# Optimization experiments

Measured on AMD Instinct MI355X. Metric: run time of the kernel, lower is better.

Reference implementation:

```python
import jax, jax.numpy as jnp
import numpy as np

N, E, D = 100000, 640000, 128

def setup_inputs() -> dict:
    key = jax.random.key(0)
    ks = jax.random.split(key, 12)
    s = 1.0 / np.sqrt(D)
    sg = 1.0 / np.sqrt(2 * D)
    return {
        "nodes": jax.random.normal(ks[0], (N, D), jnp.float32),
        "globals_": jax.random.normal(ks[1], (1, D), jnp.float32),
        "senders": jax.random.randint(ks[2], (E,), 0, N, jnp.int32),
        "receivers": jax.random.randint(ks[3], (E,), 0, N, jnp.int32),
        "W1_w": jax.random.normal(ks[4], (D, D), jnp.float32) * s,
        "W1_b": jnp.zeros((D,), jnp.float32),
        "W2_w": jax.random.normal(ks[5], (D, D), jnp.float32) * s,
        "W2_b": jnp.zeros((D,), jnp.float32),
        "W3_w": jax.random.normal(ks[6], (D, D), jnp.float32) * s,
        "W3_b": jnp.zeros((D,), jnp.float32),
        "Wg_w": jax.random.normal(ks[7], (2 * D, D), jnp.float32) * sg,
        "Wg_b": jnp.zeros((D,), jnp.float32),
    }


def reference(nodes, globals_, senders, receivers,
              W1_w, W1_b, W2_w, W2_b, W3_w, W3_b, Wg_w, Wg_b):
    n = nodes.shape[0]
    # W1 skip-branch projection
    h = nodes @ W1_w + W1_b                              # [N, D]
    # GraphConvolution: W2 projection + symmetric-normalized sum aggregation
    conv = nodes @ W2_w + W2_b                           # [N, D]
    ones = jnp.ones(senders.shape, conv.dtype)
    send_deg = jax.ops.segment_sum(ones, senders, num_segments=n)
    recv_deg = jax.ops.segment_sum(ones, receivers, num_segments=n)
    conv = conv * jax.lax.rsqrt(jnp.maximum(send_deg, 1.0))[:, None]
    agg = jax.ops.segment_sum(conv[senders], receivers, num_segments=n)  # gather + scatter
    agg = agg * jax.lax.rsqrt(jnp.maximum(recv_deg, 1.0))[:, None]
    h = h + agg
    # global -> node broadcast (globals is not None)
    h = h + (globals_[0:1] @ W3_w + W3_b)
    h = jax.nn.relu(h)
    h = h + nodes                                        # residual
    # global update: aggregate nodes (sum over single graph) + gated residual
    an = jnp.sum(h, axis=0, keepdims=True)               # [1, D]
    g_new = globals_ + jax.nn.relu(jnp.concatenate([an, globals_], axis=-1) @ Wg_w + Wg_b)
    return h, g_new
```

## Files before the change

kernel.cpp:

```cpp
#include <hip/hip_runtime.h>

#define D 128
#define AGGB 2048
#define MAXDEG 16
#define OVFCAP 16384

typedef __attribute__((ext_vector_type(8))) short short8;
typedef __attribute__((ext_vector_type(4))) float floatx4;

__device__ inline void bf16split(float x, ushort& hi, ushort& lo) {
  unsigned u = __float_as_uint(x);
  unsigned rh = (u + 0x7FFFu + ((u >> 16) & 1u)) & 0xFFFF0000u;
  hi = (ushort)(rh >> 16);
  float fl = x - __uint_as_float(rh);
  unsigned ul = __float_as_uint(fl);
  lo = (ushort)((ul + 0x7FFFu + ((ul >> 16) & 1u)) >> 16);
}

__global__ void k_front(const int* __restrict__ snd, const int* __restrict__ rcv,
                        int* __restrict__ cs, int* __restrict__ cr,
                        int* __restrict__ srtp, int* __restrict__ ovf,
                        int* __restrict__ ovfn, int E, int nbE,
                        const float* __restrict__ g, const float* __restrict__ W3,
                        const float* __restrict__ b3, float* __restrict__ gvec,
                        const float* __restrict__ W1, const float* __restrict__ W2,
                        ushort* __restrict__ wt) {
  __shared__ float part[256];
  const int b = blockIdx.x;
  if (b < nbE) {
    const int e = b * 256 + threadIdx.x;
    if (e < E) {
      const int s = snd[e], r = rcv[e];
      atomicAdd(cs + s, 1);
      const int p = atomicAdd(cr + r, 1);
      if (p < MAXDEG) {
        srtp[r * MAXDEG + p] = s;
      } else {
        const int q = atomicAdd(ovfn, 1);
        if (q < OVFCAP) {
          ovf[2 * q] = r;
          ovf[2 * q + 1] = s;
        }
      }
    }
    return;
  }
  if (b == nbE) {
    const int j = threadIdx.x & 127, half = threadIdx.x >> 7;
    float acc = 0.f;
    for (int k = half * 64; k < half * 64 + 64; ++k)
      acc = fmaf(g[k], W3[k * D + j], acc);
    part[threadIdx.x] = acc;
    __syncthreads();
    if (threadIdx.x < D) gvec[j] = b3[j] + part[j] + part[j + 128];
    return;
  }
  const int id = (b - nbE - 1) * 256 + threadIdx.x;
  const int mat = id >> 14, idx = id & 16383;
  const int k = idx >> 7, nn = idx & 127;
  const float x = (mat ? W2 : W1)[k * D + nn];
  ushort hi, lo;
  bf16split(x, hi, lo);
  wt[(size_t)mat * 32768 + (size_t)nn * 128 + k] = hi;
  wt[(size_t)mat * 32768 + 16384 + (size_t)nn * 128 + k] = lo;
}

__global__ __launch_bounds__(256) void k_agg(
    const float* __restrict__ nodes, int* __restrict__ cnt_recv,
    const int* __restrict__ cnt_send, const int* __restrict__ srtp,
    const int* __restrict__ ovf, const int* __restrict__ ovfn,
    ushort* __restrict__ yh, ushort* __restrict__ yl, int n) {
  float* cf = (float*)cnt_recv;
  const int hw = threadIdx.x >> 5, ln = threadIdx.x & 31;
  const int ghw = blockIdx.x * 8 + hw;
  const int nhw = AGGB * 8;
  const int c0 = ln * 4;

  for (int r0 = ghw; r0 < n; r0 += 2 * nhw) {
    const int r1 = r0 + nhw;
    const bool has1 = r1 < n;
    const int dg0 = cnt_recv[r0];
    const int dg1 = has1 ? cnt_recv[r1] : 0;
    const int base0 = r0 * MAXDEG;
    const int base1 = (has1 ? r1 : 0) * MAXDEG;

    int idx0[8], idx1[8];
#pragma unroll
    for (int j = 0; j < 8; ++j) {
      const int raw0 = srtp[base0 + j];
      const int raw1 = srtp[base1 + j];
      idx0[j] = (j < dg0) ? raw0 : 0;
      idx1[j] = (j < dg1) ? raw1 : 0;
    }
    float4 g0[8], g1[8];
#pragma unroll
    for (int j = 0; j < 8; ++j)
      g0[j] = *(const float4*)(nodes + (size_t)idx0[j] * D + c0);
#pragma unroll
    for (int j = 0; j < 8; ++j)
      g1[j] = *(const float4*)(nodes + (size_t)idx1[j] * D + c0);
    float rs0[8], rs1[8];
#pragma unroll
    for (int j = 0; j < 8; ++j) {
      rs0[j] = (j < dg0) ? rsqrtf(fmaxf((float)cnt_send[idx0[j]], 1.f)) : 0.f;
      rs1[j] = (j < dg1) ? rsqrtf(fmaxf((float)cnt_send[idx1[j]], 1.f)) : 0.f;
    }

    float sx0 = 0.f, sy0 = 0.f, sz0 = 0.f, sw0 = 0.f, cs0 = 0.f;
    float sx1 = 0.f, sy1 = 0.f, sz1 = 0.f, sw1 = 0.f, cs1 = 0.f;
#pragma unroll
    for (int j = 0; j < 8; ++j) {
      sx0 = fmaf(rs0[j], g0[j].x, sx0);
      sy0 = fmaf(rs0[j], g0[j].y, sy0);
      sz0 = fmaf(rs0[j], g0[j].z, sz0);
      sw0 = fmaf(rs0[j], g0[j].w, sw0);
      cs0 += rs0[j];
      sx1 = fmaf(rs1[j], g1[j].x, sx1);
      sy1 = fmaf(rs1[j], g1[j].y, sy1);
      sz1 = fmaf(rs1[j], g1[j].z, sz1);
      sw1 = fmaf(rs1[j], g1[j].w, sw1);
      cs1 += rs1[j];
    }
    for (int i = 8; i < min(dg0, MAXDEG); ++i) {
      const int s = srtp[base0 + i];
      const float r = rsqrtf(fmaxf((float)cnt_send[s], 1.f));
      const float4 c = *(const float4*)(nodes + (size_t)s * D + c0);
      sx0 = fmaf(r, c.x, sx0); sy0 = fmaf(r, c.y, sy0);
      sz0 = fmaf(r, c.z, sz0); sw0 = fmaf(r, c.w, sw0);
      cs0 += r;
    }
    for (int i = 8; i < min(dg1, MAXDEG); ++i) {
      const int s = srtp[base1 + i];
      const float r = rsqrtf(fmaxf((float)cnt_send[s], 1.f));
      const float4 c = *(const float4*)(nodes + (size_t)s * D + c0);
      sx1 = fmaf(r, c.x, sx1); sy1 = fmaf(r, c.y, sy1);
      sz1 = fmaf(r, c.z, sz1); sw1 = fmaf(r, c.w, sw1);
      cs1 += r;
    }
    if (dg0 > MAXDEG) {
      const int novf = min(*ovfn, OVFCAP);
      for (int k2 = 0; k2 < novf; ++k2) {
        if (ovf[2 * k2] == r0) {
          const int s = ovf[2 * k2 + 1];
          const float r = rsqrtf(fmaxf((float)cnt_send[s], 1.f));
          const float4 c = *(const float4*)(nodes + (size_t)s * D + c0);
          sx0 = fmaf(r, c.x, sx0); sy0 = fmaf(r, c.y, sy0);
          sz0 = fmaf(r, c.z, sz0); sw0 = fmaf(r, c.w, sw0);
          cs0 += r;
        }
      }
    }
    if (dg1 > MAXDEG) {
      const int novf = min(*ovfn, OVFCAP);
      for (int k2 = 0; k2 < novf; ++k2) {
        if (ovf[2 * k2] == r1) {
          const int s = ovf[2 * k2 + 1];
          const float r = rsqrtf(fmaxf((float)cnt_send[s], 1.f));
          const float4 c = *(const float4*)(nodes + (size_t)s * D + c0);
          sx1 = fmaf(r, c.x, sx1); sy1 = fmaf(r, c.y, sy1);
          sz1 = fmaf(r, c.z, sz1); sw1 = fmaf(r, c.w, sw1);
          cs1 += r;
        }
      }
    }

    {
      const float rr = rsqrtf(fmaxf((float)dg0, 1.f));
      ushort h0, l0, h1, l1, h2, l2, h3, l3;
      bf16split(sx0 * rr, h0, l0);
      bf16split(sy0 * rr, h1, l1);
      bf16split(sz0 * rr, h2, l2);
      bf16split(sw0 * rr, h3, l3);
      *(ushort4*)(yh + (size_t)r0 * D + c0) = make_ushort4(h0, h1, h2, h3);
      *(ushort4*)(yl + (size_t)r0 * D + c0) = make_ushort4(l0, l1, l2, l3);
      if (ln == 0) cf[r0] = rr * cs0;
    }
    if (has1) {
      const float rr = rsqrtf(fmaxf((float)dg1, 1.f));
      ushort h0, l0, h1, l1, h2, l2, h3, l3;
      bf16split(sx1 * rr, h0, l0);
      bf16split(sy1 * rr, h1, l1);
      bf16split(sz1 * rr, h2, l2);
      bf16split(sw1 * rr, h3, l3);
      *(ushort4*)(yh + (size_t)r1 * D + c0) = make_ushort4(h0, h1, h2, h3);
      *(ushort4*)(yl + (size_t)r1 * D + c0) = make_ushort4(l0, l1, l2, l3);
      if (ln == 0) cf[r1] = rr * cs1;
    }
  }
}

__global__ __launch_bounds__(256, 4) void k_gemm(
    const float* __restrict__ A, const ushort* __restrict__ yh,
    const ushort* __restrict__ yl, const ushort* __restrict__ wt,
    const float* __restrict__ b1, const float* __restrict__ b2,
    const float* __restrict__ gvec, const float* __restrict__ cf,
    float* __restrict__ outH, float* __restrict__ an, int n) {
  __shared__ ushort As[2 * 4 * 2560];
  const int t = threadIdx.x;
  const int row0 = blockIdx.x * 64;
  const int lane = t & 63, w = t >> 6;
  const int m = lane & 15, quad = lane >> 4;

  floatx4 acc[4][2];
#pragma unroll
  for (int i = 0; i < 4; ++i)
#pragma unroll
    for (int j = 0; j < 2; ++j) acc[i][j] = (floatx4)0.f;

  const int srow = t >> 2, ko = (t & 3) * 8;
  const int grow = min(row0 + srow, n - 1);
  const float* Ag = A + (size_t)grow * D + ko;
  const ushort* yhb = yh + (size_t)grow * D + ko;
  const ushort* ylb = yl + (size_t)grow * D + ko;
  const int sa = srow * 40 + ko;

  float4 f0, f1;
  uint4 r2, r3;
#define LOADP(p)                                  \
  {                                               \
    f0 = *(const float4*)(Ag + (p) * 32);         \
    f1 = *(const float4*)(Ag + (p) * 32 + 4);     \
    r2 = *(const uint4*)(yhb + (p) * 32);         \
    r3 = *(const uint4*)(ylb + (p) * 32);         \
  }
#define STOREB(buf)                                                        \
  {                                                                        \
    ushort h0, l0, h1, l1, h2, l2, h3, l3;                                 \
    ushort* Bp = &As[(buf) * 10240];                                       \
    bf16split(f0.x, h0, l0); bf16split(f0.y, h1, l1);                      \
    bf16split(f0.z, h2, l2); bf16split(f0.w, h3, l3);                      \
    *(ushort4*)&Bp[sa] = make_ushort4(h0, h1, h2, h3);                     \
    *(ushort4*)&Bp[2560 + sa] = make_ushort4(l0, l1, l2, l3);              \
    bf16split(f1.x, h0, l0); bf16split(f1.y, h1, l1);                      \
    bf16split(f1.z, h2, l2); bf16split(f1.w, h3, l3);                      \
    *(ushort4*)&Bp[sa + 4] = make_ushort4(h0, h1, h2, h3);                 \
    *(ushort4*)&Bp[2560 + sa + 4] = make_ushort4(l0, l1, l2, l3);          \
    *(uint4*)&Bp[5120 + sa] = r2;                                          \
    *(uint4*)&Bp[7680 + sa] = r3;                                          \
  }

  LOADP(0);
  STOREB(0);
  LOADP(1);
  __syncthreads();

  for (int p = 0; p < 4; ++p) {
    if (p < 3) STOREB((p + 1) & 1);
    if (p < 2) LOADP(p + 2);
    const ushort* Ab = &As[(p & 1) * 10240];
#pragma unroll
    for (int j = 0; j < 2; ++j) {
      const ushort* g1 = wt + (size_t)(w * 32 + j * 16 + m) * 128 + p * 32 + quad * 8;
      const short8 w1h = *(const short8*)g1;
      const short8 w1l = *(const short8*)(g1 + 16384);
      const short8 w2h = *(const short8*)(g1 + 32768);
      const short8 w2l = *(const short8*)(g1 + 49152);
#pragma unroll
      for (int i = 0; i < 4; ++i) {
        const int r = (i * 16 + m) * 40 + quad * 8;
        const short8 a1h = *(const short8*)&Ab[r];
        const short8 a1l = *(const short8*)&Ab[2560 + r];
        const short8 a2h = *(const short8*)&Ab[5120 + r];
        const short8 a2l = *(const short8*)&Ab[7680 + r];
        floatx4 c = acc[i][j];
        c = __builtin_amdgcn_mfma_f32_16x16x32_bf16(a1h, w1h, c, 0, 0, 0);
        c = __builtin_amdgcn_mfma_f32_16x16x32_bf16(a1h, w1l, c, 0, 0, 0);
        c = __builtin_amdgcn_mfma_f32_16x16x32_bf16(a1l, w1h, c, 0, 0, 0);
        c = __builtin_amdgcn_mfma_f32_16x16x32_bf16(a2h, w2h, c, 0, 0, 0);
        c = __builtin_amdgcn_mfma_f32_16x16x32_bf16(a2h, w2l, c, 0, 0, 0);
        c = __builtin_amdgcn_mfma_f32_16x16x32_bf16(a2l, w2h, c, 0, 0, 0);
        acc[i][j] = c;
      }
    }
    __syncthreads();
  }
#undef LOADP
#undef STOREB

  float bb[2], b2c[2];
#pragma unroll
  for (int j = 0; j < 2; ++j) {
    const int col = w * 32 + j * 16 + m;
    bb[j] = b1[col] + gvec[col];
    b2c[j] = b2[col];
  }
  float asum[2] = {0.f, 0.f};
#pragma unroll
  for (int i = 0; i < 4; ++i)
#pragma unroll
    for (int pp = 0; pp < 4; ++pp) {
      const int rg = row0 + i * 16 + quad * 4 + pp;
      if (rg >= n) continue;
      const float crv = cf[rg];
#pragma unroll
      for (int j = 0; j < 2; ++j) {
        const int col = w * 32 + j * 16 + m;
        float v = acc[i][j][pp] + bb[j] + crv * b2c[j];
        v = fmaxf(v, 0.f) + A[(size_t)rg * D + col];
        outH[(size_t)rg * D + col] = v;
        asum[j] += v;
      }
    }
#pragma unroll
  for (int j = 0; j < 2; ++j) {
    float v = asum[j];
    v += __shfl_xor(v, 16);
    v += __shfl_xor(v, 32);
    if (lane < 16) atomicAdd(an + w * 32 + j * 16 + m, v);
  }
}

__global__ void k_gupdate(const float* __restrict__ an, const float* __restrict__ g,
                          const float* __restrict__ Wg, const float* __restrict__ bg,
                          float* __restrict__ gout) {
  __shared__ float part[256];
  const int j = threadIdx.x & 127, half = threadIdx.x >> 7;
  float acc = 0.f;
  if (half == 0) {
    for (int k = 0; k < D; ++k) acc = fmaf(an[k], Wg[k * D + j], acc);
  } else {
    for (int k = 0; k < D; ++k) acc = fmaf(g[k], Wg[(D + k) * D + j], acc);
  }
  part[threadIdx.x] = acc;
  __syncthreads();
  if (threadIdx.x < D)
    gout[j] = g[j] + fmaxf(bg[j] + part[j] + part[j + 128], 0.f);
}

extern "C" void kernel_launch(void* const* d_in, const int* in_sizes, int n_in,
                              void* d_out, int out_size, void* d_ws, size_t ws_size,
                              hipStream_t stream) {
  const float* nodes = (const float*)d_in[0];
  const float* globals_ = (const float*)d_in[1];
  const int* senders = (const int*)d_in[2];
  const int* receivers = (const int*)d_in[3];
  const float* W1_w = (const float*)d_in[4];
  const float* W1_b = (const float*)d_in[5];
  const float* W2_w = (const float*)d_in[6];
  const float* W2_b = (const float*)d_in[7];
  const float* W3_w = (const float*)d_in[8];
  const float* W3_b = (const float*)d_in[9];
  const float* Wg_w = (const float*)d_in[10];
  const float* Wg_b = (const float*)d_in[11];
  const int N = in_sizes[0] / D;
  const int E = in_sizes[2];
  const int nbE = (E + 255) / 256;

  float* h = (float*)d_out;
  float* gout = h + (size_t)N * D;

  float* ws = (float*)d_ws;
  ushort* yh = (ushort*)ws;
  ushort* yl = yh + (size_t)N * D;
  int* cnt_send = (int*)(yl + (size_t)N * D);
  int* cnt_recv = cnt_send + N;
  float* an = (float*)(cnt_recv + N);
  int* ovfn = (int*)(an + D);
  float* gvec = (float*)(ovfn + 64);
  int* srtp = (int*)(gvec + D);
  int* ovf = srtp + (size_t)N * MAXDEG;
  ushort* wt = (ushort*)(ovf + 2 * OVFCAP);

  (void)hipMemsetAsync(cnt_send, 0, (size_t)(2 * N + D + 64) * sizeof(int), stream);

  hipLaunchKernelGGL(k_front, dim3(nbE + 1 + 128), dim3(256), 0, stream,
                     senders, receivers, cnt_send, cnt_recv, srtp, ovf, ovfn,
                     E, nbE, globals_, W3_w, W3_b, gvec, W1_w, W2_w, wt);
  hipLaunchKernelGGL(k_agg, dim3(AGGB), dim3(256), 0, stream,
                     nodes, cnt_recv, cnt_send, srtp, ovf, ovfn, yh, yl, N);
  hipLaunchKernelGGL(k_gemm, dim3((N + 63) / 64), dim3(256), 0, stream,
                     nodes, yh, yl, wt, W1_b, W2_b, gvec,
                     (const float*)cnt_recv, h, an, N);
  hipLaunchKernelGGL(k_gupdate, dim3(1), dim3(256), 0, stream, an, globals_,
                     Wg_w, Wg_b, gout);
}
```

Before: 350.2 us.

## Overlap W1 projection GEMM with edge counting and split GEMM into two passes

```diff
diff --git a/kernel.cpp b/kernel.cpp
--- a/kernel.cpp
+++ b/kernel.cpp
@@ -1,7 +1,7 @@
 #include <hip/hip_runtime.h>
 
 #define D 128
-#define AGGB 2048
+#define AGGB 3136
 #define MAXDEG 16
 #define OVFCAP 16384
 
@@ -17,35 +17,26 @@
   lo = (ushort)((ul + 0x7FFFu + ((ul >> 16) & 1u)) >> 16);
 }
 
-__global__ void k_front(const int* __restrict__ snd, const int* __restrict__ rcv,
-                        int* __restrict__ cs, int* __restrict__ cr,
-                        int* __restrict__ srtp, int* __restrict__ ovf,
-                        int* __restrict__ ovfn, int E, int nbE,
-                        const float* __restrict__ g, const float* __restrict__ W3,
-                        const float* __restrict__ b3, float* __restrict__ gvec,
-                        const float* __restrict__ W1, const float* __restrict__ W2,
-                        ushort* __restrict__ wt) {
-  __shared__ float part[256];
+__device__ inline void place_edge(int s, int r, int p, int* __restrict__ srtp,
+                                  int* __restrict__ ovf, int* __restrict__ ovfn) {
+  if (p < MAXDEG) {
+    srtp[r * MAXDEG + p] = s;
+  } else {
+    const int q = atomicAdd(ovfn, 1);
+    if (q < OVFCAP) {
+      ovf[2 * q] = r;
+      ovf[2 * q + 1] = s;
+    }
+  }
+}
+
+__global__ void k_prep(const float* __restrict__ g, const float* __restrict__ W3,
+                       const float* __restrict__ b3, float* __restrict__ gvec,
+                       const float* __restrict__ W1, const float* __restrict__ W2,
+                       ushort* __restrict__ wt) {
   const int b = blockIdx.x;
-  if (b < nbE) {
-    const int e = b * 256 + threadIdx.x;
-    if (e < E) {
-      const int s = snd[e], r = rcv[e];
-      atomicAdd(cs + s, 1);
-      const int p = atomicAdd(cr + r, 1);
-      if (p < MAXDEG) {
-        srtp[r * MAXDEG + p] = s;
-      } else {
-        const int q = atomicAdd(ovfn, 1);
-        if (q < OVFCAP) {
-          ovf[2 * q] = r;
-          ovf[2 * q + 1] = s;
-        }
-      }
-    }
-    return;
-  }
-  if (b == nbE) {
+  if (b == 0) {
+    __shared__ float part[256];
     const int j = threadIdx.x & 127, half = threadIdx.x >> 7;
     float acc = 0.f;
     for (int k = half * 64; k < half * 64 + 64; ++k)
@@ -55,7 +46,7 @@
     if (threadIdx.x < D) gvec[j] = b3[j] + part[j] + part[j + 128];
     return;
   }
-  const int id = (b - nbE - 1) * 256 + threadIdx.x;
+  const int id = (b - 1) * 256 + threadIdx.x;
   const int mat = id >> 14, idx = id & 16383;
   const int k = idx >> 7, nn = idx & 127;
   const float x = (mat ? W2 : W1)[k * D + nn];
@@ -63,6 +54,118 @@
   bf16split(x, hi, lo);
   wt[(size_t)mat * 32768 + (size_t)nn * 128 + k] = hi;
   wt[(size_t)mat * 32768 + 16384 + (size_t)nn * 128 + k] = lo;
+}
+
+__global__ __launch_bounds__(256, 6) void k_eg(
+    const int* __restrict__ snd, const int* __restrict__ rcv,
+    int* __restrict__ cs, int* __restrict__ cr, int* __restrict__ srtp,
+    int* __restrict__ ovf, int* __restrict__ ovfn, int E, int nbE4,
+    const float* __restrict__ A, const ushort* __restrict__ wt,
+    float* __restrict__ h1, int n) {
+  const int b = blockIdx.x, t = threadIdx.x;
+  if (b < nbE4) {
+    const int e0 = b * 1024 + t * 4;
+    if (e0 + 3 < E) {
+      const int4 s4 = *(const int4*)(snd + e0);
+      const int4 r4 = *(const int4*)(rcv + e0);
+      atomicAdd(cs + s4.x, 1);
+      atomicAdd(cs + s4.y, 1);
+      atomicAdd(cs + s4.z, 1);
+      atomicAdd(cs + s4.w, 1);
+      const int p0 = atomicAdd(cr + r4.x, 1);
+      const int p1 = atomicAdd(cr + r4.y, 1);
+      const int p2 = atomicAdd(cr + r4.z, 1);
+      const int p3 = atomicAdd(cr + r4.w, 1);
+      place_edge(s4.x, r4.x, p0, srtp, ovf, ovfn);
+      place_edge(s4.y, r4.y, p1, srtp, ovf, ovfn);
+      place_edge(s4.z, r4.z, p2, srtp, ovf, ovfn);
+      place_edge(s4.w, r4.w, p3, srtp, ovf, ovfn);
+    } else {
+      for (int e = e0; e < E && e < e0 + 4; ++e) {
+        const int s = snd[e], r = rcv[e];
+        atomicAdd(cs + s, 1);
+        place_edge(s, r, atomicAdd(cr + r, 1), srtp, ovf, ovfn);
+      }
+    }
+    return;
+  }
+  __shared__ ushort As[2 * 2 * 2560];
+  const int row0 = (b - nbE4) * 64;
+  const int lane = t & 63, w = t >> 6;
+  const int m = lane & 15, quad = lane >> 4;
+
+  floatx4 acc[4][2];
+#pragma unroll
+  for (int i = 0; i < 4; ++i)
+#pragma unroll
+    for (int j = 0; j < 2; ++j) acc[i][j] = (floatx4)0.f;
+
+  const int srow = t >> 2, ko = (t & 3) * 8;
+  const int grow = min(row0 + srow, n - 1);
+  const float* Ag = A + (size_t)grow * D + ko;
+  const int sa = srow * 40 + ko;
+
+  float4 f0, f1;
+#define LOADP(p)                              \
+  {                                           \
+    f0 = *(const float4*)(Ag + (p) * 32);     \
+    f1 = *(const float4*)(Ag + (p) * 32 + 4); \
+  }
+#define STOREB(buf)                                               \
+  {                                                               \
+    ushort h0, l0, h1_, l1_, h2, l2, h3, l3;                      \
+    ushort* Bp = &As[(buf) * 5120];                               \
+    bf16split(f0.x, h0, l0); bf16split(f0.y, h1_, l1_);           \
+    bf16split(f0.z, h2, l2); bf16split(f0.w, h3, l3);             \
+    *(ushort4*)&Bp[sa] = make_ushort4(h0, h1_, h2, h3);           \
+    *(ushort4*)&Bp[2560 + sa] = make_ushort4(l0, l1_, l2, l3);    \
+    bf16split(f1.x, h0, l0); bf16split(f1.y, h1_, l1_);           \
+    bf16split(f1.z, h2, l2); bf16split(f1.w, h3, l3);             \
+    *(ushort4*)&Bp[sa + 4] = make_ushort4(h0, h1_, h2, h3);       \
+    *(ushort4*)&Bp[2560 + sa + 4] = make_ushort4(l0, l1_, l2, l3);\
+  }
+
+  LOADP(0);
+  STOREB(0);
+  LOADP(1);
+  __syncthreads();
+
+  for (int p = 0; p < 4; ++p) {
+    if (p < 3) STOREB((p + 1) & 1);
+    if (p < 2) LOADP(p + 2);
+    const ushort* Ab = &As[(p & 1) * 5120];
+#pragma unroll
+    for (int j = 0; j < 2; ++j) {
+      const ushort* g1 = wt + (size_t)(w * 32 + j * 16 + m) * 128 + p * 32 + quad * 8;
+      const short8 w1h = *(const short8*)g1;
+      const short8 w1l = *(const short8*)(g1 + 16384);
+#pragma unroll
+      for (int i = 0; i < 4; ++i) {
+        const int r = (i * 16 + m) * 40 + quad * 8;
+        const short8 a1h = *(const short8*)&Ab[r];
+        const short8 a1l = *(const short8*)&Ab[2560 + r];
+        floatx4 c = acc[i][j];
+        c = __builtin_amdgcn_mfma_f32_16x16x32_bf16(a1h, w1h, c, 0, 0, 0);
+        c = __builtin_amdgcn_mfma_f32_16x16x32_bf16(a1h, w1l, c, 0, 0, 0);
+        c = __builtin_amdgcn_mfma_f32_16x16x32_bf16(a1l, w1h, c, 0, 0, 0);
+        acc[i][j] = c;
+      }
+    }
+    __syncthreads();
+  }
+#undef LOADP
+#undef STOREB
+
+#pragma unroll
+  for (int i = 0; i < 4; ++i)
+#pragma unroll
+    for (int pp = 0; pp < 4; ++pp) {
+      const int rg = row0 + i * 16 + quad * 4 + pp;
+      if (rg >= n) continue;
+#pragma unroll
+      for (int j = 0; j < 2; ++j)
+        h1[(size_t)rg * D + w * 32 + j * 16 + m] = acc[i][j][pp];
+    }
 }
 
 __global__ __launch_bounds__(256) void k_agg(
@@ -84,13 +187,16 @@
     const int base0 = r0 * MAXDEG;
     const int base1 = (has1 ? r1 : 0) * MAXDEG;
 
-    int idx0[8], idx1[8];
+    const int4 qa0 = *(const int4*)(srtp + base0);
+    const int4 qb0 = *(const int4*)(srtp + base0 + 4);
+    const int4 qa1 = *(const int4*)(srtp + base1);
+    const int4 qb1 = *(const int4*)(srtp + base1 + 4);
+    int idx0[8] = {qa0.x, qa0.y, qa0.z, qa0.w, qb0.x, qb0.y, qb0.z, qb0.w};
+    int idx1[8] = {qa1.x, qa1.y, qa1.z, qa1.w, qb1.x, qb1.y, qb1.z, qb1.w};
 #pragma unroll
     for (int j = 0; j < 8; ++j) {
-      const int raw0 = srtp[base0 + j];
-      const int raw1 = srtp[base1 + j];
-      idx0[j] = (j < dg0) ? raw0 : 0;
-      idx1[j] = (j < dg1) ? raw1 : 0;
+      idx0[j] = (j < dg0) ? idx0[j] : 0;
+      idx1[j] = (j < dg1) ? idx1[j] : 0;
     }
     float4 g0[8], g1[8];
 #pragma unroll
@@ -189,13 +295,13 @@
   }
 }
 
-__global__ __launch_bounds__(256, 4) void k_gemm(
+__global__ __launch_bounds__(256, 6) void k_gemm2(
     const float* __restrict__ A, const ushort* __restrict__ yh,
     const ushort* __restrict__ yl, const ushort* __restrict__ wt,
     const float* __restrict__ b1, const float* __restrict__ b2,
     const float* __restrict__ gvec, const float* __restrict__ cf,
-    float* __restrict__ outH, float* __restrict__ an, int n) {
-  __shared__ ushort As[2 * 4 * 2560];
+    float* hio, float* __restrict__ an, int n) {
+  __shared__ ushort As[2 * 2 * 2560];
   const int t = threadIdx.x;
   const int row0 = blockIdx.x * 64;
   const int lane = t & 63, w = t >> 6;
@@ -209,34 +315,21 @@
 
   const int srow = t >> 2, ko = (t & 3) * 8;
   const int grow = min(row0 + srow, n - 1);
-  const float* Ag = A + (size_t)grow * D + ko;
   const ushort* yhb = yh + (size_t)grow * D + ko;
   const ushort* ylb = yl + (size_t)grow * D + ko;
   const int sa = srow * 40 + ko;
 
-  float4 f0, f1;
   uint4 r2, r3;
-#define LOADP(p)                                  \
-  {                                               \
-    f0 = *(const float4*)(Ag + (p) * 32);         \
-    f1 = *(const float4*)(Ag + (p) * 32 + 4);     \
-    r2 = *(const uint4*)(yhb + (p) * 32);         \
-    r3 = *(const uint4*)(ylb + (p) * 32);         \
-  }
-#define STOREB(buf)                                                        \
-  {                                                                        \
-    ushort h0, l0, h1, l1, h2, l2, h3, l3;                                 \
-    ushort* Bp = &As[(buf) * 10240];                                       \
-    bf16split(f0.x, h0, l0); bf16split(f0.y, h1, l1);                      \
-    bf16split(f0.z, h2, l2); bf16split(f0.w, h3, l3);                      \
-    *(ushort4*)&Bp[sa] = make_ushort4(h0, h1, h2, h3);                     \
-    *(ushort4*)&Bp[2560 + sa] = make_ushort4(l0, l1, l2, l3);              \
-    bf16split(f1.x, h0, l0); bf16split(f1.y, h1, l1);                      \
-    bf16split(f1.z, h2, l2); bf16split(f1.w, h3, l3);                      \
-    *(ushort4*)&Bp[sa + 4] = make_ushort4(h0, h1, h2, h3);                 \
-    *(ushort4*)&Bp[2560 + sa + 4] = make_ushort4(l0, l1, l2, l3);          \
-    *(uint4*)&Bp[5120 + sa] = r2;                                          \
-    *(uint4*)&Bp[7680 + sa] = r3;                                          \
+#define LOADP(p)                          \
+  {                                       \
+    r2 = *(const uint4*)(yhb + (p) * 32); \
+    r3 = *(const uint4*)(ylb + (p) * 32); \
+  }
+#define STOREB(buf)                 \
+  {                                 \
+    ushort* Bp = &As[(buf) * 5120]; \
+    *(uint4*)&Bp[sa] = r2;          \
+    *(uint4*)&Bp[2560 + sa] = r3;   \
   }
 
   LOADP(0);
@@ -247,25 +340,19 @@
   for (int p = 0; p < 4; ++p) {
     if (p < 3) STOREB((p + 1) & 1);
     if (p < 2) LOADP(p + 2);
-    const ushort* Ab = &As[(p & 1) * 10240];
+    const ushort* Ab = &As[(p & 1) * 5120];
 #pragma unroll
     for (int j = 0; j < 2; ++j) {
-      const ushort* g1 = wt + (size_t)(w * 32 + j * 16 + m) * 128 + p * 32 + quad * 8;
-      const short8 w1h = *(const short8*)g1;
-      const short8 w1l = *(const short8*)(g1 + 16384);
-      const short8 w2h = *(const short8*)(g1 + 32768);
-      const short8 w2l = *(const short8*)(g1 + 49152);
+      const ushort* g2 =
+          wt + 32768 + (size_t)(w * 32 + j * 16 + m) * 128 + p * 32 + quad * 8;
+      const short8 w2h = *(const short8*)g2;
+      const short8 w2l = *(const short8*)(g2 + 16384);
 #pragma unroll
       for (int i = 0; i < 4; ++i) {
         const int r = (i * 16 + m) * 40 + quad * 8;
-        const short8 a1h = *(const short8*)&Ab[r];
-        const short8 a1l = *(const short8*)&Ab[2560 + r];
-        const short8 a2h = *(const short8*)&Ab[5120 + r];
-        const short8 a2l = *(const short8*)&Ab[7680 + r];
+        const short8 a2h = *(const short8*)&Ab[r];
+        const short8 a2l = *(const short8*)&Ab[2560 + r];
         floatx4 c = acc[i][j];
-        c = __builtin_amdgcn_mfma_f32_16x16x32_bf16(a1h, w1h, c, 0, 0, 0);
-        c = __builtin_amdgcn_mfma_f32_16x16x32_bf16(a1h, w1l, c, 0, 0, 0);
-        c = __builtin_amdgcn_mfma_f32_16x16x32_bf16(a1l, w1h, c, 0, 0, 0);
         c = __builtin_amdgcn_mfma_f32_16x16x32_bf16(a2h, w2h, c, 0, 0, 0);
         c = __builtin_amdgcn_mfma_f32_16x16x32_bf16(a2h, w2l, c, 0, 0, 0);
         c = __builtin_amdgcn_mfma_f32_16x16x32_bf16(a2l, w2h, c, 0, 0, 0);
@@ -295,9 +382,9 @@
 #pragma unroll
       for (int j = 0; j < 2; ++j) {
         const int col = w * 32 + j * 16 + m;
-        float v = acc[i][j][pp] + bb[j] + crv * b2c[j];
+        float v = acc[i][j][pp] + bb[j] + crv * b2c[j] + hio[(size_t)rg * D + col];
         v = fmaxf(v, 0.f) + A[(size_t)rg * D + col];
-        outH[(size_t)rg * D + col] = v;
+        hio[(size_t)rg * D + col] = v;
         asum[j] += v;
       }
     }
@@ -344,7 +431,8 @@
   const float* Wg_b = (const float*)d_in[11];
   const int N = in_sizes[0] / D;
   const int E = in_sizes[2];
-  const int nbE = (E + 255) / 256;
+  const int nbE4 = (E + 1023) / 1024;
+  const int NG = (N + 63) / 64;
 
   float* h = (float*)d_out;
   float* gout = h + (size_t)N * D;
@@ -363,12 +451,14 @@
 
   (void)hipMemsetAsync(cnt_send, 0, (size_t)(2 * N + D + 64) * sizeof(int), stream);
 
-  hipLaunchKernelGGL(k_front, dim3(nbE + 1 + 128), dim3(256), 0, stream,
+  hipLaunchKernelGGL(k_prep, dim3(129), dim3(256), 0, stream,
+                     globals_, W3_w, W3_b, gvec, W1_w, W2_w, wt);
+  hipLaunchKernelGGL(k_eg, dim3(nbE4 + NG), dim3(256), 0, stream,
                      senders, receivers, cnt_send, cnt_recv, srtp, ovf, ovfn,
-                     E, nbE, globals_, W3_w, W3_b, gvec, W1_w, W2_w, wt);
+                     E, nbE4, nodes, wt, h, N);
   hipLaunchKernelGGL(k_agg, dim3(AGGB), dim3(256), 0, stream,
                      nodes, cnt_recv, cnt_send, srtp, ovf, ovfn, yh, yl, N);
-  hipLaunchKernelGGL(k_gemm, dim3((N + 63) / 64), dim3(256), 0, stream,
+  hipLaunchKernelGGL(k_gemm2, dim3(NG), dim3(256), 0, stream,
                      nodes, yh, yl, wt, W1_b, W2_b, gvec,
                      (const float*)cnt_recv, h, an, N);
   hipLaunchKernelGGL(k_gupdate, dim3(1), dim3(256), 0, stream, an, globals_,
```

Result: slower. 376.5 us (+7.5%).

## Fuse neighbor aggregation into GEMM tile kernel and vectorize edge binning

Applied to the files above, without the earlier changes.

```diff
diff --git a/kernel.cpp b/kernel.cpp
--- a/kernel.cpp
+++ b/kernel.cpp
@@ -1,7 +1,6 @@
 #include <hip/hip_runtime.h>
 
 #define D 128
-#define AGGB 2048
 #define MAXDEG 16
 #define OVFCAP 16384
 
@@ -17,45 +16,66 @@
   lo = (ushort)((ul + 0x7FFFu + ((ul >> 16) & 1u)) >> 16);
 }
 
+__device__ inline void place_edge(int s, int r, int p, int* __restrict__ srtp,
+                                  int* __restrict__ ovf, int* __restrict__ ovfn) {
+  if (p < MAXDEG) {
+    srtp[r * MAXDEG + p] = s;
+  } else {
+    const int q = atomicAdd(ovfn, 1);
+    if (q < OVFCAP) {
+      ovf[2 * q] = r;
+      ovf[2 * q + 1] = s;
+    }
+  }
+}
+
 __global__ void k_front(const int* __restrict__ snd, const int* __restrict__ rcv,
                         int* __restrict__ cs, int* __restrict__ cr,
                         int* __restrict__ srtp, int* __restrict__ ovf,
-                        int* __restrict__ ovfn, int E, int nbE,
+                        int* __restrict__ ovfn, int E, int nbE4,
                         const float* __restrict__ g, const float* __restrict__ W3,
                         const float* __restrict__ b3, float* __restrict__ gvec,
                         const float* __restrict__ W1, const float* __restrict__ W2,
                         ushort* __restrict__ wt) {
-  __shared__ float part[256];
-  const int b = blockIdx.x;
-  if (b < nbE) {
-    const int e = b * 256 + threadIdx.x;
-    if (e < E) {
-      const int s = snd[e], r = rcv[e];
-      atomicAdd(cs + s, 1);
-      const int p = atomicAdd(cr + r, 1);
-      if (p < MAXDEG) {
-        srtp[r * MAXDEG + p] = s;
-      } else {
-        const int q = atomicAdd(ovfn, 1);
-        if (q < OVFCAP) {
-          ovf[2 * q] = r;
-          ovf[2 * q + 1] = s;
-        }
+  const int b = blockIdx.x, t = threadIdx.x;
+  if (b < nbE4) {
+    const int e0 = b * 1024 + t * 4;
+    if (e0 + 3 < E) {
+      const int4 s4 = *(const int4*)(snd + e0);
+      const int4 r4 = *(const int4*)(rcv + e0);
+      atomicAdd(cs + s4.x, 1);
+      atomicAdd(cs + s4.y, 1);
+      atomicAdd(cs + s4.z, 1);
+      atomicAdd(cs + s4.w, 1);
+      const int p0 = atomicAdd(cr + r4.x, 1);
+      const int p1 = atomicAdd(cr + r4.y, 1);
+      const int p2 = atomicAdd(cr + r4.z, 1);
+      const int p3 = atomicAdd(cr + r4.w, 1);
+      place_edge(s4.x, r4.x, p0, srtp, ovf, ovfn);
+      place_edge(s4.y, r4.y, p1, srtp, ovf, ovfn);
+      place_edge(s4.z, r4.z, p2, srtp, ovf, ovfn);
+      place_edge(s4.w, r4.w, p3, srtp, ovf, ovfn);
+    } else {
+      for (int e = e0; e < E && e < e0 + 4; ++e) {
+        const int s = snd[e], r = rcv[e];
+        atomicAdd(cs + s, 1);
+        place_edge(s, r, atomicAdd(cr + r, 1), srtp, ovf, ovfn);
       }
     }
     return;
   }
-  if (b == nbE) {
-    const int j = threadIdx.x & 127, half = threadIdx.x >> 7;
+  if (b == nbE4) {
+    __shared__ float part[256];
+    const int j = t & 127, half = t >> 7;
     float acc = 0.f;
     for (int k = half * 64; k < half * 64 + 64; ++k)
       acc = fmaf(g[k], W3[k * D + j], acc);
-    part[threadIdx.x] = acc;
+    part[t] = acc;
     __syncthreads();
-    if (threadIdx.x < D) gvec[j] = b3[j] + part[j] + part[j + 128];
+    if (t < D) gvec[j] = b3[j] + part[j] + part[j + 128];
     return;
   }
-  const int id = (b - nbE - 1) * 256 + threadIdx.x;
+  const int id = (b - nbE4 - 1) * 256 + t;
   const int mat = id >> 14, idx = id & 16383;
   const int k = idx >> 7, nn = idx & 127;
   const float x = (mat ? W2 : W1)[k * D + nn];
@@ -65,203 +85,176 @@
   wt[(size_t)mat * 32768 + 16384 + (size_t)nn * 128 + k] = lo;
 }
 
-__global__ __launch_bounds__(256) void k_agg(
-    const float* __restrict__ nodes, int* __restrict__ cnt_recv,
-    const int* __restrict__ cnt_send, const int* __restrict__ srtp,
+__global__ __launch_bounds__(256, 3) void k_ag2(
+    const float* __restrict__ nodes, const int* __restrict__ cr,
+    const int* __restrict__ cs, const int* __restrict__ srtp,
     const int* __restrict__ ovf, const int* __restrict__ ovfn,
-    ushort* __restrict__ yh, ushort* __restrict__ yl, int n) {
-  float* cf = (float*)cnt_recv;
-  const int hw = threadIdx.x >> 5, ln = threadIdx.x & 31;
-  const int ghw = blockIdx.x * 8 + hw;
-  const int nhw = AGGB * 8;
-  const int c0 = ln * 4;
-
-  for (int r0 = ghw; r0 < n; r0 += 2 * nhw) {
-    const int r1 = r0 + nhw;
-    const bool has1 = r1 < n;
-    const int dg0 = cnt_recv[r0];
-    const int dg1 = has1 ? cnt_recv[r1] : 0;
-    const int base0 = r0 * MAXDEG;
-    const int base1 = (has1 ? r1 : 0) * MAXDEG;
-
-    int idx0[8], idx1[8];
-#pragma unroll
-    for (int j = 0; j < 8; ++j) {
-      const int raw0 = srtp[base0 + j];
-      const int raw1 = srtp[base1 + j];
-      idx0[j] = (j < dg0) ? raw0 : 0;
-      idx1[j] = (j < dg1) ? raw1 : 0;
-    }
-    float4 g0[8], g1[8];
-#pragma unroll
-    for (int j = 0; j < 8; ++j)
-      g0[j] = *(const float4*)(nodes + (size_t)idx0[j] * D + c0);
-#pragma unroll
-    for (int j = 0; j < 8; ++j)
-      g1[j] = *(const float4*)(nodes + (size_t)idx1[j] * D + c0);
-    float rs0[8], rs1[8];
-#pragma unroll
-    for (int j = 0; j < 8; ++j) {
-      rs0[j] = (j < dg0) ? rsqrtf(fmaxf((float)cnt_send[idx0[j]], 1.f)) : 0.f;
-      rs1[j] = (j < dg1) ? rsqrtf(fmaxf((float)cnt_send[idx1[j]], 1.f)) : 0.f;
-    }
-
-    float sx0 = 0.f, sy0 = 0.f, sz0 = 0.f, sw0 = 0.f, cs0 = 0.f;
-    float sx1 = 0.f, sy1 = 0.f, sz1 = 0.f, sw1 = 0.f, cs1 = 0.f;
-#pragma unroll
-    for (int j = 0; j < 8; ++j) {
-      sx0 = fmaf(rs0[j], g0[j].x, sx0);
-      sy0 = fmaf(rs0[j], g0[j].y, sy0);
-      sz0 = fmaf(rs0[j], g0[j].z, sz0);
-      sw0 = fmaf(rs0[j], g0[j].w, sw0);
-      cs0 += rs0[j];
-      sx1 = fmaf(rs1[j], g1[j].x, sx1);
-      sy1 = fmaf(rs1[j], g1[j].y, sy1);
-      sz1 = fmaf(rs1[j], g1[j].z, sz1);
-      sw1 = fmaf(rs1[j], g1[j].w, sw1);
-      cs1 += rs1[j];
-    }
-    for (int i = 8; i < min(dg0, MAXDEG); ++i) {
-      const int s = srtp[base0 + i];
-      const float r = rsqrtf(fmaxf((float)cnt_send[s], 1.f));
-      const float4 c = *(const float4*)(nodes + (size_t)s * D + c0);
-      sx0 = fmaf(r, c.x, sx0); sy0 = fmaf(r, c.y, sy0);
-      sz0 = fmaf(r, c.z, sz0); sw0 = fmaf(r, c.w, sw0);
-      cs0 += r;
-    }
-    for (int i = 8; i < min(dg1, MAXDEG); ++i) {
-      const int s = srtp[base1 + i];
-      const float r = rsqrtf(fmaxf((float)cnt_send[s], 1.f));
-      const float4 c = *(const float4*)(nodes + (size_t)s * D + c0);
-      sx1 = fmaf(r, c.x, sx1); sy1 = fmaf(r, c.y, sy1);
-      sz1 = fmaf(r, c.z, sz1); sw1 = fmaf(r, c.w, sw1);
-      cs1 += r;
-    }
-    if (dg0 > MAXDEG) {
-      const int novf = min(*ovfn, OVFCAP);
-      for (int k2 = 0; k2 < novf; ++k2) {
-        if (ovf[2 * k2] == r0) {
-          const int s = ovf[2 * k2 + 1];
-          const float r = rsqrtf(fmaxf((float)cnt_send[s], 1.f));
-          const float4 c = *(const float4*)(nodes + (size_t)s * D + c0);
-          sx0 = fmaf(r, c.x, sx0); sy0 = fmaf(r, c.y, sy0);
-          sz0 = fmaf(r, c.z, sz0); sw0 = fmaf(r, c.w, sw0);
-          cs0 += r;
-        }
-      }
-    }
-    if (dg1 > MAXDEG) {
-      const int novf = min(*ovfn, OVFCAP);
-      for (int k2 = 0; k2 < novf; ++k2) {
-        if (ovf[2 * k2] == r1) {
-          const int s = ovf[2 * k2 + 1];
-          const float r = rsqrtf(fmaxf((float)cnt_send[s], 1.f));
-          const float4 c = *(const float4*)(nodes + (size_t)s * D + c0);
-          sx1 = fmaf(r, c.x, sx1); sy1 = fmaf(r, c.y, sy1);
-          sz1 = fmaf(r, c.z, sz1); sw1 = fmaf(r, c.w, sw1);
-          cs1 += r;
-        }
-      }
-    }
-
-    {
-      const float rr = rsqrtf(fmaxf((float)dg0, 1.f));
-      ushort h0, l0, h1, l1, h2, l2, h3, l3;
-      bf16split(sx0 * rr, h0, l0);
-      bf16split(sy0 * rr, h1, l1);
-      bf16split(sz0 * rr, h2, l2);
-      bf16split(sw0 * rr, h3, l3);
-      *(ushort4*)(yh + (size_t)r0 * D + c0) = make_ushort4(h0, h1, h2, h3);
-      *(ushort4*)(yl + (size_t)r0 * D + c0) = make_ushort4(l0, l1, l2, l3);
-      if (ln == 0) cf[r0] = rr * cs0;
-    }
-    if (has1) {
-      const float rr = rsqrtf(fmaxf((float)dg1, 1.f));
-      ushort h0, l0, h1, l1, h2, l2, h3, l3;
-      bf16split(sx1 * rr, h0, l0);
-      bf16split(sy1 * rr, h1, l1);
-      bf16split(sz1 * rr, h2, l2);
-      bf16split(sw1 * rr, h3, l3);
-      *(ushort4*)(yh + (size_t)r1 * D + c0) = make_ushort4(h0, h1, h2, h3);
-      *(ushort4*)(yl + (size_t)r1 * D + c0) = make_ushort4(l0, l1, l2, l3);
-      if (ln == 0) cf[r1] = rr * cs1;
-    }
-  }
-}
-
-__global__ __launch_bounds__(256, 4) void k_gemm(
-    const float* __restrict__ A, const ushort* __restrict__ yh,
-    const ushort* __restrict__ yl, const ushort* __restrict__ wt,
-    const float* __restrict__ b1, const float* __restrict__ b2,
-    const float* __restrict__ gvec, const float* __restrict__ cf,
-    float* __restrict__ outH, float* __restrict__ an, int n) {
-  __shared__ ushort As[2 * 4 * 2560];
+    const ushort* __restrict__ wt, const float* __restrict__ b1,
+    const float* __restrict__ b2, const float* __restrict__ gvec,
+    float* __restrict__ h, float* __restrict__ an, int n) {
+  __shared__ ushort As[4 * 5120];
+  __shared__ float cfl[32];
   const int t = threadIdx.x;
-  const int row0 = blockIdx.x * 64;
+  const int row0 = blockIdx.x * 32;
+
+  {
+    const int hw = t >> 5, ln = t & 31;
+    const int c0 = ln * 4;
+    const int sl = ln >> 3;
+    const int kk = (ln & 7) * 4;
+    const int sb = sl * 1280 + kk;
+
+    for (int it = 0; it < 2; ++it) {
+      const int lrA = hw + it * 8;
+      const int lrB = lrA + 16;
+      const int rA = row0 + lrA, rB = row0 + lrB;
+      const bool hasA = rA < n, hasB = rB < n;
+      const int dgA = hasA ? cr[rA] : 0;
+      const int dgB = hasB ? cr[rB] : 0;
+      const int baseA = (hasA ? rA : 0) * MAXDEG;
+      const int baseB = (hasB ? rB : 0) * MAXDEG;
+
+      const int4 qa0 = *(const int4*)(srtp + baseA);
+      const int4 qb0 = *(const int4*)(srtp + baseA + 4);
+      const int4 qa1 = *(const int4*)(srtp + baseB);
+      const int4 qb1 = *(const int4*)(srtp + baseB + 4);
+      int idxA[8] = {qa0.x, qa0.y, qa0.z, qa0.w, qb0.x, qb0.y, qb0.z, qb0.w};
+      int idxB[8] = {qa1.x, qa1.y, qa1.z, qa1.w, qb1.x, qb1.y, qb1.z, qb1.w};
+#pragma unroll
+      for (int j = 0; j < 8; ++j) {
+        idxA[j] = (j < dgA) ? idxA[j] : 0;
+        idxB[j] = (j < dgB) ? idxB[j] : 0;
+      }
+      float4 gA[8], gB[8];
+#pragma unroll
+      for (int j = 0; j < 8; ++j)
+        gA[j] = *(const float4*)(nodes + (size_t)idxA[j] * D + c0);
+#pragma unroll
+      for (int j = 0; j < 8; ++j)
+        gB[j] = *(const float4*)(nodes + (size_t)idxB[j] * D + c0);
+      const float4 ndA = hasA ? *(const float4*)(nodes + (size_t)rA * D + c0)
+                              : make_float4(0.f, 0.f, 0.f, 0.f);
+      const float4 ndB = hasB ? *(const float4*)(nodes + (size_t)rB * D + c0)
+                              : make_float4(0.f, 0.f, 0.f, 0.f);
+      float rsA[8], rsB[8];
+#pragma unroll
+      for (int j = 0; j < 8; ++j) {
+        rsA[j] = (j < dgA) ? rsqrtf(fmaxf((float)cs[idxA[j]], 1.f)) : 0.f;
+        rsB[j] = (j < dgB) ? rsqrtf(fmaxf((float)cs[idxB[j]], 1.f)) : 0.f;
+      }
+      float sxA = 0.f, syA = 0.f, szA = 0.f, swA = 0.f, csA = 0.f;
+      float sxB = 0.f, syB = 0.f, szB = 0.f, swB = 0.f, csB = 0.f;
+#pragma unroll
+      for (int j = 0; j < 8; ++j) {
+        sxA = fmaf(rsA[j], gA[j].x, sxA);
+        syA = fmaf(rsA[j], gA[j].y, syA);
+        szA = fmaf(rsA[j], gA[j].z, szA);
+        swA = fmaf(rsA[j], gA[j].w, swA);
+        csA += rsA[j];
+        sxB = fmaf(rsB[j], gB[j].x, sxB);
+        syB = fmaf(rsB[j], gB[j].y, syB);
+        szB = fmaf(rsB[j], gB[j].z, szB);
+        swB = fmaf(rsB[j], gB[j].w, swB);
+        csB += rsB[j];
+      }
+      for (int i = 8; i < min(dgA, MAXDEG); ++i) {
+        const int s = srtp[baseA + i];
+        const float r = rsqrtf(fmaxf((float)cs[s], 1.f));
+        const float4 c = *(const float4*)(nodes + (size_t)s * D + c0);
+        sxA = fmaf(r, c.x, sxA); syA = fmaf(r, c.y, syA);
+        szA = fmaf(r, c.z, szA); swA = fmaf(r, c.w, swA);
+        csA += r;
+      }
+      for (int i = 8; i < min(dgB, MAXDEG); ++i) {
+        const int s = srtp[baseB + i];
+        const float r = rsqrtf(fmaxf((float)cs[s], 1.f));
+        const float4 c = *(const float4*)(nodes + (size_t)s * D + c0);
+        sxB = fmaf(r, c.x, sxB); syB = fmaf(r, c.y, syB);
+        szB = fmaf(r, c.z, szB); swB = fmaf(r, c.w, swB);
+        csB += r;
+      }
+      if (dgA > MAXDEG) {
+        const int novf = min(*ovfn, OVFCAP);
+        for (int k2 = 0; k2 < novf; ++k2)
+          if (ovf[2 * k2] == rA) {
+            const int s = ovf[2 * k2 + 1];
+            const float r = rsqrtf(fmaxf((float)cs[s], 1.f));
+            const float4 c = *(const float4*)(nodes + (size_t)s * D + c0);
+            sxA = fmaf(r, c.x, sxA); syA = fmaf(r, c.y, syA);
+            szA = fmaf(r, c.z, szA); swA = fmaf(r, c.w, swA);
+            csA += r;
+          }
+      }
+      if (dgB > MAXDEG) {
+        const int novf = min(*ovfn, OVFCAP);
+        for (int k2 = 0; k2 < novf; ++k2)
+          if (ovf[2 * k2] == rB) {
+            const int s = ovf[2 * k2 + 1];
+            const float r = rsqrtf(fmaxf((float)cs[s], 1.f));
+            const float4 c = *(const float4*)(nodes + (size_t)s * D + c0);
+            sxB = fmaf(r, c.x, sxB); syB = fmaf(r, c.y, syB);
+            szB = fmaf(r, c.z, szB); swB = fmaf(r, c.w, swB);
+            csB += r;
+          }
+      }
+      if (hasA) {
+        const float rr = rsqrtf(fmaxf((float)dgA, 1.f));
+        ushort h0, l0, h1, l1, h2, l2, h3, l3;
+        const int a = sb + lrA * 40;
+        bf16split(ndA.x, h0, l0); bf16split(ndA.y, h1, l1);
+        bf16split(ndA.z, h2, l2); bf16split(ndA.w, h3, l3);
+        *(ushort4*)&As[a] = make_ushort4(h0, h1, h2, h3);
+        *(ushort4*)&As[5120 + a] = make_ushort4(l0, l1, l2, l3);
+        bf16split(sxA * rr, h0, l0); bf16split(syA * rr, h1, l1);
+        bf16split(szA * rr, h2, l2); bf16split(swA * rr, h3, l3);
+        *(ushort4*)&As[10240 + a] = make_ushort4(h0, h1, h2, h3);
+        *(ushort4*)&As[15360 + a] = make_ushort4(l0, l1, l2, l3);
+        if (ln == 0) cfl[lrA] = rr * csA;
+      }
+      if (hasB) {
+        const float rr = rsqrtf(fmaxf((float)dgB, 1.f));
+        ushort h0, l0, h1, l1, h2, l2, h3, l3;
+        const int a = sb + lrB * 40;
+        bf16split(ndB.x, h0, l0); bf16split(ndB.y, h1, l1);
+        bf16split(ndB.z, h2, l2); bf16split(ndB.w, h3, l3);
+        *(ushort4*)&As[a] = make_ushort4(h0, h1, h2, h3);
+        *(ushort4*)&As[5120 + a] = make_ushort4(l0, l1, l2, l3);
+        bf16split(sxB * rr, h0, l0); bf16split(syB * rr, h1, l1);
+        bf16split(szB * rr, h2, l2); bf16split(swB * rr, h3, l3);
+        *(ushort4*)&As[10240 + a] = make_ushort4(h0, h1, h2, h3);
+        *(ushort4*)&As[15360 + a] = make_ushort4(l0, l1, l2, l3);
+        if (ln == 0) cfl[lrB] = rr * csB;
+      }
+    }
+  }
+  __syncthreads();
+
   const int lane = t & 63, w = t >> 6;
   const int m = lane & 15, quad = lane >> 4;
 
-  floatx4 acc[4][2];
-#pragma unroll
-  for (int i = 0; i < 4; ++i)
+  floatx4 acc[2][2];
+#pragma unroll
+  for (int i = 0; i < 2; ++i)
 #pragma unroll
     for (int j = 0; j < 2; ++j) acc[i][j] = (floatx4)0.f;
 
-  const int srow = t >> 2, ko = (t & 3) * 8;
-  const int grow = min(row0 + srow, n - 1);
-  const float* Ag = A + (size_t)grow * D + ko;
-  const ushort* yhb = yh + (size_t)grow * D + ko;
-  const ushort* ylb = yl + (size_t)grow * D + ko;
-  const int sa = srow * 40 + ko;
-
-  float4 f0, f1;
-  uint4 r2, r3;
-#define LOADP(p)                                  \
-  {                                               \
-    f0 = *(const float4*)(Ag + (p) * 32);         \
-    f1 = *(const float4*)(Ag + (p) * 32 + 4);     \
-    r2 = *(const uint4*)(yhb + (p) * 32);         \
-    r3 = *(const uint4*)(ylb + (p) * 32);         \
-  }
-#define STOREB(buf)                                                        \
-  {                                                                        \
-    ushort h0, l0, h1, l1, h2, l2, h3, l3;                                 \
-    ushort* Bp = &As[(buf) * 10240];                                       \
-    bf16split(f0.x, h0, l0); bf16split(f0.y, h1, l1);                      \
-    bf16split(f0.z, h2, l2); bf16split(f0.w, h3, l3);                      \
-    *(ushort4*)&Bp[sa] = make_ushort4(h0, h1, h2, h3);                     \
-    *(ushort4*)&Bp[2560 + sa] = make_ushort4(l0, l1, l2, l3);              \
-    bf16split(f1.x, h0, l0); bf16split(f1.y, h1, l1);                      \
-    bf16split(f1.z, h2, l2); bf16split(f1.w, h3, l3);                      \
-    *(ushort4*)&Bp[sa + 4] = make_ushort4(h0, h1, h2, h3);                 \
-    *(ushort4*)&Bp[2560 + sa + 4] = make_ushort4(l0, l1, l2, l3);          \
-    *(uint4*)&Bp[5120 + sa] = r2;                                          \
-    *(uint4*)&Bp[7680 + sa] = r3;                                          \
-  }
-
-  LOADP(0);
-  STOREB(0);
-  LOADP(1);
-  __syncthreads();
-
+#pragma unroll
   for (int p = 0; p < 4; ++p) {
-    if (p < 3) STOREB((p + 1) & 1);
-    if (p < 2) LOADP(p + 2);
-    const ushort* Ab = &As[(p & 1) * 10240];
 #pragma unroll
     for (int j = 0; j < 2; ++j) {
-      const ushort* g1 = wt + (size_t)(w * 32 + j * 16 + m) * 128 + p * 32 + quad * 8;
+      const ushort* g1 =
+          wt + (size_t)(w * 32 + j * 16 + m) * 128 + p * 32 + quad * 8;
       const short8 w1h = *(const short8*)g1;
       const short8 w1l = *(const short8*)(g1 + 16384);
       const short8 w2h = *(const short8*)(g1 + 32768);
       const short8 w2l = *(const short8*)(g1 + 49152);
 #pragma unroll
-      for (int i = 0; i < 4; ++i) {
-        const int r = (i * 16 + m) * 40 + quad * 8;
-        const short8 a1h = *(const short8*)&Ab[r];
-        const short8 a1l = *(const short8*)&Ab[2560 + r];
-        const short8 a2h = *(const short8*)&Ab[5120 + r];
-        const short8 a2l = *(const short8*)&Ab[7680 + r];
+      for (int i = 0; i < 2; ++i) {
+        const int off = p * 1280 + (i * 16 + m) * 40 + quad * 8;
+        const short8 a1h = *(const short8*)&As[off];
+        const short8 a1l = *(const short8*)&As[5120 + off];
+        const short8 a2h = *(const short8*)&As[10240 + off];
+        const short8 a2l = *(const short8*)&As[15360 + off];
         floatx4 c = acc[i][j];
         c = __builtin_amdgcn_mfma_f32_16x16x32_bf16(a1h, w1h, c, 0, 0, 0);
         c = __builtin_amdgcn_mfma_f32_16x16x32_bf16(a1h, w1l, c, 0, 0, 0);
@@ -272,10 +265,7 @@
         acc[i][j] = c;
       }
     }
-    __syncthreads();
-  }
-#undef LOADP
-#undef STOREB
+  }
 
   float bb[2], b2c[2];
 #pragma unroll
@@ -286,18 +276,19 @@
   }
   float asum[2] = {0.f, 0.f};
 #pragma unroll
-  for (int i = 0; i < 4; ++i)
+  for (int i = 0; i < 2; ++i)
 #pragma unroll
     for (int pp = 0; pp < 4; ++pp) {
-      const int rg = row0 + i * 16 + quad * 4 + pp;
+      const int lr = i * 16 + quad * 4 + pp;
+      const int rg = row0 + lr;
       if (rg >= n) continue;
-      const float crv = cf[rg];
+      const float crv = cfl[lr];
 #pragma unroll
       for (int j = 0; j < 2; ++j) {
         const int col = w * 32 + j * 16 + m;
         float v = acc[i][j][pp] + bb[j] + crv * b2c[j];
-        v = fmaxf(v, 0.f) + A[(size_t)rg * D + col];
-        outH[(size_t)rg * D + col] = v;
+        v = fmaxf(v, 0.f) + nodes[(size_t)rg * D + col];
+        h[(size_t)rg * D + col] = v;
         asum[j] += v;
       }
     }
@@ -344,33 +335,30 @@
   const float* Wg_b = (const float*)d_in[11];
   const int N = in_sizes[0] / D;
   const int E = in_sizes[2];
-  const int nbE = (E + 255) / 256;
+  const int nbE4 = (E + 1023) / 1024;
+  const int nTile = (N + 31) / 32;
 
   float* h = (float*)d_out;
   float* gout = h + (size_t)N * D;
 
   float* ws = (float*)d_ws;
-  ushort* yh = (ushort*)ws;
-  ushort* yl = yh + (size_t)N * D;
-  int* cnt_send = (int*)(yl + (size_t)N * D);
-  int* cnt_recv = cnt_send + N;
-  float* an = (float*)(cnt_recv + N);
+  int* cs = (int*)ws;
+  int* cr = cs + N;
+  float* an = (float*)(cr + N);
   int* ovfn = (int*)(an + D);
   float* gvec = (float*)(ovfn + 64);
   int* srtp = (int*)(gvec + D);
   int* ovf = srtp + (size_t)N * MAXDEG;
   ushort* wt = (ushort*)(ovf + 2 * OVFCAP);
 
-  (void)hipMemsetAsync(cnt_send, 0, (size_t)(2 * N + D + 64) * sizeof(int), stream);
-
-  hipLaunchKernelGGL(k_front, dim3(nbE + 1 + 128), dim3(256), 0, stream,
-                     senders, receivers, cnt_send, cnt_recv, srtp, ovf, ovfn,
-                     E, nbE, globals_, W3_w, W3_b, gvec, W1_w, W2_w, wt);
-  hipLaunchKernelGGL(k_agg, dim3(AGGB), dim3(256), 0, stream,
-                     nodes, cnt_recv, cnt_send, srtp, ovf, ovfn, yh, yl, N);
-  hipLaunchKernelGGL(k_gemm, dim3((N + 63) / 64), dim3(256), 0, stream,
-                     nodes, yh, yl, wt, W1_b, W2_b, gvec,
-                     (const float*)cnt_recv, h, an, N);
+  (void)hipMemsetAsync(cs, 0, (size_t)(2 * N + D + 64) * sizeof(int), stream);
+
+  hipLaunchKernelGGL(k_front, dim3(nbE4 + 1 + 128), dim3(256), 0, stream,
+                     senders, receivers, cs, cr, srtp, ovf, ovfn, E, nbE4,
+                     globals_, W3_w, W3_b, gvec, W1_w, W2_w, wt);
+  hipLaunchKernelGGL(k_ag2, dim3(nTile), dim3(256), 0, stream,
+                     nodes, cr, cs, srtp, ovf, ovfn, wt, W1_b, W2_b, gvec,
+                     h, an, N);
   hipLaunchKernelGGL(k_gupdate, dim3(1), dim3(256), 0, stream, an, globals_,
                      Wg_w, Wg_b, gout);
 }
```

Measured after the change: 342.3 us. -2.2%, faster.
